# Performance work log

Measured on AMD Instinct MI355X. Metric: run time of the kernel, lower is better.

The kernel has to match this reference:

```python
import jax, jax.numpy as jnp
import numpy as np

EMBED_DIM = 512
NUM_HEADS = 8
HEAD_DIM = EMBED_DIM // NUM_HEADS
REL_MAX = 16
NUM_POS_IDS = 2 * REL_MAX + 1 + 1  # 34 (directed + padding id)
PADDING_IDX = 0
B, S = 2, 2048


def setup_inputs() -> dict:
    key = jax.random.key(0)
    ks = jax.random.split(key, 9)
    Q = jax.random.normal(ks[0], (B, S, EMBED_DIM), dtype=jnp.float32)
    K = jax.random.normal(ks[1], (B, S, EMBED_DIM), dtype=jnp.float32)
    V = jax.random.normal(ks[2], (B, S, EMBED_DIM), dtype=jnp.float32)
    rel_pos_ids = jax.random.randint(ks[3], (B, S, S), 0, NUM_POS_IDS, dtype=jnp.int64) if jax.config.jax_enable_x64 else jax.random.randint(ks[3], (B, S, S), 0, NUM_POS_IDS, dtype=jnp.int32)
    scale = 0.02
    Wq = jax.random.normal(ks[4], (EMBED_DIM, EMBED_DIM), dtype=jnp.float32) * scale
    Wk = jax.random.normal(ks[5], (EMBED_DIM, EMBED_DIM), dtype=jnp.float32) * scale
    Wv = jax.random.normal(ks[6], (EMBED_DIM, EMBED_DIM), dtype=jnp.float32) * scale
    Wo = jax.random.normal(ks[7], (EMBED_DIM, EMBED_DIM), dtype=jnp.float32) * scale
    rel_emb = jax.random.normal(ks[8], (NUM_POS_IDS, EMBED_DIM), dtype=jnp.float32) * scale
    rel_emb = rel_emb.at[PADDING_IDX].set(0.0)  # nn.Embedding padding_idx row is zero
    return {"Q": Q, "K": K, "V": V, "rel_pos_ids": rel_pos_ids,
            "Wq": Wq, "Wk": Wk, "Wv": Wv, "Wo": Wo, "rel_emb": rel_emb}


def _proj(x, W):
    # Linear (no bias) then strided head split: view(B, S, head_dim, H) -> (B, H, S, head_dim)
    b, s, _ = x.shape
    y = x @ W.T
    return y.reshape(b, s, HEAD_DIM, NUM_HEADS).transpose(0, 3, 1, 2)


def _forward(Q, K, V, rel_pos_ids, Wq, Wk, Wv, Wo, rel_emb):
    b, sq, _ = Q.shape
    Qp = _proj(Q, Wq)  # (B, H, Sq, hd)
    Kp = _proj(K, Wk)  # (B, H, Sk, hd)
    Vp = _proj(V, Wv)  # (B, H, Sk, hd)

    # rel_embeds split per head with the same strided layout: (P, hd, H) -> (H, P, hd)
    R = rel_emb.reshape(NUM_POS_IDS, HEAD_DIM, NUM_HEADS).transpose(2, 0, 1)
    # Q_rel: (B, H, Sq, P)
    Q_rel = jnp.einsum('bhsd,hpd->bhsp', Qp, R)
    # gather per-pair relative bias: (B, H, Sq, Sk)
    rel_shift = jnp.take_along_axis(Q_rel, rel_pos_ids[:, None, :, :], axis=3)
    mask = (rel_pos_ids == PADDING_IDX)[:, None, :, :]
    rel_shift = jnp.where(mask, -jnp.inf, rel_shift)

    energy = (jnp.einsum('bhqd,bhkd->bhqk', Qp, Kp) + rel_shift) / jnp.sqrt(jnp.float32(HEAD_DIM))
    attn = jax.nn.softmax(energy, axis=-1)
    out = jnp.einsum('bhqk,bhkd->bhqd', attn, Vp)  # (B, H, Sq, hd)
    # inverse of strided split: (B, Sq, hd, H) -> flatten last two
    out = out.transpose(0, 2, 3, 1).reshape(b, sq, EMBED_DIM)
    return out @ Wo.T


def reference(Q, K, V, rel_pos_ids, Wq, Wk, Wv, Wo, rel_emb):
    return _forward(Q, K, V, rel_pos_ids, Wq, Wk, Wv, Wo, rel_emb)
```

## Files before the change

kernel.cpp:

```cpp
#include <hip/hip_runtime.h>
#include <cstdint>
#include <cstddef>

#define SEQ   2048
#define BBAT  2
#define EMBED 512
#define NH    8
#define HD    64
#define NPOS  34

typedef __bf16 bf16;
typedef __bf16 bf16x8 __attribute__((ext_vector_type(8)));
typedef float  f32x4  __attribute__((ext_vector_type(4)));
typedef int    int32x4 __attribute__((ext_vector_type(4)));

#define ESCALE 0.1803368801111204f

__device__ __forceinline__ f32x4 mfma16(bf16x8 a, bf16x8 b, f32x4 c){
  return __builtin_amdgcn_mfma_f32_16x16x32_bf16(a, b, c, 0, 0, 0);
}

__device__ __forceinline__ void barrier_lgkm(){
  asm volatile("s_waitcnt lgkmcnt(0)" ::: "memory");
  __builtin_amdgcn_s_barrier();
  __builtin_amdgcn_sched_barrier(0);
}

__global__ __launch_bounds__(256) void k_prep(
    const float* __restrict__ Q, const float* __restrict__ K, const float* __restrict__ V,
    const float* __restrict__ Wq, const float* __restrict__ Wk,
    const float* __restrict__ Wv, const float* __restrict__ Wo,
    const float* __restrict__ RE,
    bf16* __restrict__ Qb, bf16* __restrict__ Kb, bf16* __restrict__ Vb,
    bf16* __restrict__ Wall, bf16* __restrict__ Rb)
{
  const int NCONV = 3*524288;
  const int NW = 196608, NO = 262144;
  int i = blockIdx.x*256 + threadIdx.x;
  if (i < NCONV){
    int tsel = i >> 19, j = i & 524287;
    const float* s = tsel==0 ? Q : (tsel==1 ? K : V);
    bf16* d       = tsel==0 ? Qb : (tsel==1 ? Kb : Vb);
    float4 v = ((const float4*)s)[j];
    union { bf16 e[4]; ushort4 u; } pk;
    pk.e[0]=(bf16)v.x; pk.e[1]=(bf16)v.y; pk.e[2]=(bf16)v.z; pk.e[3]=(bf16)v.w;
    ((ushort4*)d)[j] = pk.u;
  } else {
    int j = i - NCONV;
    if (j < NW){
      int w  = j >> 16;
      int r  = j & 65535;
      int np = r >> 7, c4 = (r & 127) << 2;
      const float* W = (w==0) ? Wq : ((w==1) ? Wk : Wv);
      int src = ((np & 63) << 3) + (np >> 6);
      float4 v = *(const float4*)(W + (size_t)src*512 + c4);
      union { bf16 e[4]; ushort4 u; } pk;
      pk.e[0]=(bf16)v.x; pk.e[1]=(bf16)v.y; pk.e[2]=(bf16)v.z; pk.e[3]=(bf16)v.w;
      *(ushort4*)(Wall + (size_t)w*262144 + (size_t)np*512 + c4) = pk.u;
    } else if (j < NW + NO){
      int jj = j - NW;
      int n = jj >> 9, kp = jj & 511;
      int src = ((kp & 63) << 3) + (kp >> 6);
      Wall[(size_t)3*262144 + (size_t)n*512 + kp] = (bf16)Wo[(size_t)n*512 + src];
    } else {
      int jj = j - NW - NO;
      if (jj < 8*48*64){
        int h  = jj / (48*64);
        int r2 = jj - h*(48*64);
        int p  = r2 >> 6, dd = r2 & 63;
        float v = (p < NPOS) ? RE[(size_t)p*512 + dd*8 + h] : 0.f;
        Rb[jj] = (bf16)v;
      }
    }
  }
}

__global__ __launch_bounds__(256,2) void k_gemm_proj(
    const bf16* __restrict__ Qb, const bf16* __restrict__ Kb, const bf16* __restrict__ Vb,
    const bf16* __restrict__ W,  bf16* __restrict__ Qp, bf16* __restrict__ Kp, bf16* __restrict__ Vt)
{
  const bf16* A  = blockIdx.z==0 ? Qb : (blockIdx.z==1 ? Kb : Vb);
  const bf16* Bw = W + (size_t)blockIdx.z*262144;

  __shared__ __align__(16) bf16 As[128][72];
  __shared__ __align__(16) bf16 Bs[64][72];
  const int t = threadIdx.x;
  const int w = t >> 6, lane = t & 63, l15 = lane & 15, quad = lane >> 4;
  const int wm = (w & 1) * 64, wn = (w >> 1) * 32;
  const int m0 = blockIdx.y * 128, n0 = blockIdx.x * 64;

  f32x4 acc[4][2];
  #pragma unroll
  for (int mt=0; mt<4; ++mt)
    #pragma unroll
    for (int nt=0; nt<2; ++nt) acc[mt][nt] = (f32x4){0.f,0.f,0.f,0.f};

  for (int kt = 0; kt < 512; kt += 64){
    #pragma unroll
    for (int i = 0; i < 4; ++i){
      int lin = t + 256*i;
      int r = lin >> 3, c8 = (lin & 7) << 3;
      *(uint4*)&As[r][c8] = *(const uint4*)(A + (size_t)(m0 + r)*512 + kt + c8);
    }
    #pragma unroll
    for (int i = 0; i < 2; ++i){
      int lin = t + 256*i;
      int r = lin >> 3, c8 = (lin & 7) << 3;
      *(uint4*)&Bs[r][c8] = *(const uint4*)(Bw + (size_t)(n0 + r)*512 + kt + c8);
    }
    __syncthreads();
    #pragma unroll
    for (int ks = 0; ks < 2; ++ks){
      bf16x8 am[4], bn[2];
      #pragma unroll
      for (int x=0;x<4;++x) am[x] = *(const bf16x8*)&As[wm + x*16 + l15][ks*32 + quad*8];
      #pragma unroll
      for (int y=0;y<2;++y) bn[y] = *(const bf16x8*)&Bs[wn + y*16 + l15][ks*32 + quad*8];
      #pragma unroll
      for (int mt=0;mt<4;++mt)
        #pragma unroll
        for (int nt=0;nt<2;++nt)
          acc[mt][nt] = mfma16(am[mt], bn[nt], acc[mt][nt]);
    }
    __syncthreads();
  }

  if (blockIdx.z != 2){
    bf16* C = blockIdx.z==0 ? Qp : Kp;
    const float scl = (blockIdx.z==0) ? ESCALE : 1.0f;
    #pragma unroll
    for (int mt=0;mt<4;++mt)
      #pragma unroll
      for (int r=0;r<4;++r){
        int m = m0 + wm + mt*16 + quad*4 + r;
        #pragma unroll
        for (int nt=0;nt<2;++nt)
          C[(size_t)m*512 + n0 + wn + nt*16 + l15] = (bf16)(acc[mt][nt][r] * scl);
      }
  } else {
    bf16 (*VT)[136] = (bf16(*)[136])As;
    #pragma unroll
    for (int mt=0;mt<4;++mt)
      #pragma unroll
      for (int r=0;r<4;++r){
        int m = wm + mt*16 + quad*4 + r;
        #pragma unroll
        for (int nt=0;nt<2;++nt)
          VT[wn + nt*16 + l15][m] = (bf16)acc[mt][nt][r];
      }
    __syncthreads();
    const int h = blockIdx.x, b = m0 >> 11, s0 = m0 & 2047;
    const int n = t >> 2, c0 = (t & 3) * 32;
    bf16* dst = Vt + ((size_t)((b*NH + h)*HD + n))*SEQ + s0 + c0;
    #pragma unroll
    for (int i = 0; i < 4; ++i)
      *(uint4*)(dst + i*8) = *(const uint4*)&VT[n][c0 + i*8];
  }
}

__global__ __launch_bounds__(256,2) void k_gemm_out(
    const bf16* __restrict__ A, const bf16* __restrict__ Bw, float* __restrict__ C)
{
  __shared__ __align__(16) bf16 As[64][72];
  __shared__ __align__(16) bf16 Bs[64][72];
  const int t = threadIdx.x;
  const int w = t >> 6, lane = t & 63, l15 = lane & 15, quad = lane >> 4;
  const int wm = (w & 1) * 32, wn = (w >> 1) * 32;
  const int m0 = blockIdx.y * 64, n0 = blockIdx.x * 64;

  f32x4 acc[2][2];
  #pragma unroll
  for (int mt=0; mt<2; ++mt)
    #pragma unroll
    for (int nt=0; nt<2; ++nt) acc[mt][nt] = (f32x4){0.f,0.f,0.f,0.f};

  for (int kt = 0; kt < 512; kt += 64){
    #pragma unroll
    for (int i = 0; i < 2; ++i){
      int lin = t + 256*i;
      int r = lin >> 3, c8 = (lin & 7) << 3;
      *(uint4*)&As[r][c8] = *(const uint4*)(A  + (size_t)(m0 + r)*512 + kt + c8);
      *(uint4*)&Bs[r][c8] = *(const uint4*)(Bw + (size_t)(n0 + r)*512 + kt + c8);
    }
    __syncthreads();
    #pragma unroll
    for (int ks = 0; ks < 2; ++ks){
      bf16x8 am[2], bn[2];
      #pragma unroll
      for (int x=0;x<2;++x) am[x] = *(const bf16x8*)&As[wm + x*16 + l15][ks*32 + quad*8];
      #pragma unroll
      for (int y=0;y<2;++y) bn[y] = *(const bf16x8*)&Bs[wn + y*16 + l15][ks*32 + quad*8];
      #pragma unroll
      for (int mt=0;mt<2;++mt)
        #pragma unroll
        for (int nt=0;nt<2;++nt)
          acc[mt][nt] = mfma16(am[mt], bn[nt], acc[mt][nt]);
    }
    __syncthreads();
  }
  #pragma unroll
  for (int mt=0;mt<2;++mt)
    #pragma unroll
    for (int r=0;r<4;++r){
      int m = m0 + wm + mt*16 + quad*4 + r;
      #pragma unroll
      for (int nt=0;nt<2;++nt)
        C[(size_t)m*512 + n0 + wn + nt*16 + l15] = acc[mt][nt][r];
    }
}

__global__ __launch_bounds__(256,2) void k_attn(
    const bf16* __restrict__ Qp, const bf16* __restrict__ Kp,
    const bf16* __restrict__ Vt, const bf16* __restrict__ Rb,
    const int* __restrict__ ids, bf16* __restrict__ Out)
{
  __shared__ __align__(16) bf16 Ks[128][72];
  __shared__ __align__(16) bf16 Vs[64][136];
  __shared__ __align__(16) bf16 Ps[64][136];
  __shared__ float lutT[35][65];
  __shared__ float lsum_s[128];

  const int t = threadIdx.x;
  const int b = blockIdx.z, h = blockIdx.y;
  const int q0 = blockIdx.x * 64;
  const int w = t >> 6, lane = t & 63, l15 = lane & 15, quad = lane >> 4;
  const int qh = w & 1, kh = w >> 1;

  const size_t idb = (size_t)b*SEQ*SEQ;
  const bf16* kbase = Kp + (size_t)b*SEQ*EMBED + h*HD;
  const bf16* vbase = Vt + (size_t)(b*NH + h)*HD*SEQ;

  const int krow = t >> 3, kcol = (t & 7) << 3;
  const int vrow = t >> 4, vcol = (t & 15) << 3;

  uint4 ka0, ka1, ka2, ka3, va0, va1, va2, va3;
  uint4 kb0, kb1, kb2, kb3, vb0, vb1, vb2, vb3;
  ka0 = *(const uint4*)(kbase + (size_t)(krow     )*EMBED + kcol);
  ka1 = *(const uint4*)(kbase + (size_t)(krow + 32)*EMBED + kcol);
  ka2 = *(const uint4*)(kbase + (size_t)(krow + 64)*EMBED + kcol);
  ka3 = *(const uint4*)(kbase + (size_t)(krow + 96)*EMBED + kcol);
  va0 = *(const uint4*)(vbase + (size_t)(vrow     )*SEQ + vcol);
  va1 = *(const uint4*)(vbase + (size_t)(vrow + 16)*SEQ + vcol);
  va2 = *(const uint4*)(vbase + (size_t)(vrow + 32)*SEQ + vcol);
  va3 = *(const uint4*)(vbase + (size_t)(vrow + 48)*SEQ + vcol);

  int32x4 nid[2][4];
  #pragma unroll
  for (int mt=0; mt<2; ++mt)
    #pragma unroll
    for (int nt=0; nt<4; ++nt)
      nid[mt][nt] = *(const int32x4*)(ids + idb
          + (size_t)(q0 + qh*32 + mt*16 + l15)*SEQ
          + kh*64 + nt*16 + quad*4);

  {
    const bf16* qbrow = Qp + (size_t)(b*SEQ + q0 + w*16 + l15)*EMBED + h*HD;
    bf16x8 ab0 = *(const bf16x8*)(qbrow + quad*8);
    bf16x8 ab1 = *(const bf16x8*)(qbrow + 32 + quad*8);
    const bf16* rh = Rb + h*3072;
    #pragma unroll
    for (int nt = 0; nt < 3; ++nt){
      bf16x8 r0 = *(const bf16x8*)(rh + (nt*16 + l15)*64 + quad*8);
      bf16x8 r1 = *(const bf16x8*)(rh + (nt*16 + l15)*64 + 32 + quad*8);
      f32x4 c = (f32x4){0.f,0.f,0.f,0.f};
      c = mfma16(ab0, r0, c);
      c = mfma16(ab1, r1, c);
      int p = nt*16 + l15;
      if (p < NPOS){
        #pragma unroll
        for (int r = 0; r < 4; ++r)
          lutT[p][w*16 + quad*4 + r] = (p == 0) ? -1e30f : c[r];
      }
    }
  }

  bf16x8 bq[2][2];
  #pragma unroll
  for (int mt = 0; mt < 2; ++mt){
    const bf16* qrow = Qp + (size_t)(b*SEQ + q0 + qh*32 + mt*16 + l15)*EMBED + h*HD;
    bq[mt][0] = *(const bf16x8*)(qrow + quad*8);
    bq[mt][1] = *(const bf16x8*)(qrow + 32 + quad*8);
  }

  f32x4 acc[2][4];
  #pragma unroll
  for (int mt=0;mt<2;++mt)
    #pragma unroll
    for (int nt=0;nt<4;++nt) acc[mt][nt] = (f32x4){0.f,0.f,0.f,0.f};
  float lsum[2] = {0.f, 0.f};

#define ATTN_BODY(KT, K0,K1,K2,K3, V0,V1,V2,V3, L0,L1,L2,L3, M0,M1,M2,M3)       \
  {                                                                             \
    barrier_lgkm();              \
    *(uint4*)&Ks[krow     ][kcol] = K0;                                         \
    *(uint4*)&Ks[krow + 32][kcol] = K1;                                         \
    *(uint4*)&Ks[krow + 64][kcol] = K2;                                         \
    *(uint4*)&Ks[krow + 96][kcol] = K3;                                         \
    *(uint4*)&Vs[vrow     ][vcol] = V0;                                         \
    *(uint4*)&Vs[vrow + 16][vcol] = V1;                                         \
    *(uint4*)&Vs[vrow + 32][vcol] = V2;                                         \
    *(uint4*)&Vs[vrow + 48][vcol] = V3;                                         \
    if ((KT) < 15){                                                             \
      const bf16* kp2 = kbase + (size_t)(((KT)+1)*128)*EMBED + kcol;            \
      const bf16* vp2 = vbase + ((KT)+1)*128 + vcol;                            \
      L0 = *(const uint4*)(kp2 + (size_t)(krow     )*EMBED);                    \
      L1 = *(const uint4*)(kp2 + (size_t)(krow + 32)*EMBED);                    \
      L2 = *(const uint4*)(kp2 + (size_t)(krow + 64)*EMBED);                    \
      L3 = *(const uint4*)(kp2 + (size_t)(krow + 96)*EMBED);                    \
      M0 = *(const uint4*)(vp2 + (size_t)(vrow     )*SEQ);                      \
      M1 = *(const uint4*)(vp2 + (size_t)(vrow + 16)*SEQ);                      \
      M2 = *(const uint4*)(vp2 + (size_t)(vrow + 32)*SEQ);                      \
      M3 = *(const uint4*)(vp2 + (size_t)(vrow + 48)*SEQ);                      \
    }                                                                           \
    barrier_lgkm();                \
    float wvv[2][4][4];                                                         \
    _Pragma("unroll")                                                           \
    for (int mt = 0; mt < 2; ++mt){                                             \
      const float* lcol = &lutT[0][qh*32 + mt*16 + l15];                        \
      _Pragma("unroll")                                                         \
      for (int nt = 0; nt < 4; ++nt){                                           \
        int32x4 v = nid[mt][nt];                                                \
        wvv[mt][nt][0] = lcol[v[0] * 65];                                       \
        wvv[mt][nt][1] = lcol[v[1] * 65];                                       \
        wvv[mt][nt][2] = lcol[v[2] * 65];                                       \
        wvv[mt][nt][3] = lcol[v[3] * 65];                                       \
      }                                                                         \
    }                                                                           \
    if ((KT) < 15){                                                             \
      _Pragma("unroll")                                                         \
      for (int mt = 0; mt < 2; ++mt)                                            \
        _Pragma("unroll")                                                       \
        for (int nt = 0; nt < 4; ++nt)                                          \
          nid[mt][nt] = *(const int32x4*)(ids + idb                             \
              + (size_t)(q0 + qh*32 + mt*16 + l15)*SEQ                          \
              + (((KT)+1)*128) + kh*64 + nt*16 + quad*4);                       \
    }                                                                           \
    f32x4 sf[2][4];                                                             \
    __builtin_amdgcn_s_setprio(1);                                              \
    _Pragma("unroll")                                                           \
    for (int nt = 0; nt < 4; ++nt){                                             \
      bf16x8 ak0 = *(const bf16x8*)&Ks[kh*64 + nt*16 + l15][quad*8];            \
      bf16x8 ak1 = *(const bf16x8*)&Ks[kh*64 + nt*16 + l15][32 + quad*8];       \
      _Pragma("unroll")                                                         \
      for (int mt = 0; mt < 2; ++mt){                                           \
        f32x4 c = (f32x4){0.f,0.f,0.f,0.f};                                     \
        c = mfma16(ak0, bq[mt][0], c);                                          \
        c = mfma16(ak1, bq[mt][1], c);                                          \
        sf[mt][nt] = c;                                                         \
      }                                                                         \
    }                                                                           \
    __builtin_amdgcn_s_setprio(0);                                              \
    _Pragma("unroll")                                                           \
    for (int mt = 0; mt < 2; ++mt){                                             \
      _Pragma("unroll")                                                         \
      for (int nt = 0; nt < 4; ++nt){                                           \
        union { bf16 e[4]; uint2 u; } pk;                                       \
        float p0 = __builtin_amdgcn_exp2f(sf[mt][nt][0] + wvv[mt][nt][0]);      \
        float p1 = __builtin_amdgcn_exp2f(sf[mt][nt][1] + wvv[mt][nt][1]);      \
        float p2 = __builtin_amdgcn_exp2f(sf[mt][nt][2] + wvv[mt][nt][2]);      \
        float p3 = __builtin_amdgcn_exp2f(sf[mt][nt][3] + wvv[mt][nt][3]);      \
        pk.e[0] = (bf16)p0; pk.e[1] = (bf16)p1;                                 \
        pk.e[2] = (bf16)p2; pk.e[3] = (bf16)p3;                                 \
        lsum[mt] += (p0 + p1) + (p2 + p3);                                      \
        *(uint2*)&Ps[qh*32 + mt*16 + l15][kh*64 + nt*16 + quad*4] = pk.u;       \
      }                                                                         \
    }                                                                           \
    __builtin_amdgcn_s_setprio(1);                                              \
    _Pragma("unroll")                                                           \
    for (int ks = 0; ks < 2; ++ks){                                             \
      bf16x8 ap[2];                                                             \
      _Pragma("unroll")                                                         \
      for (int mt = 0; mt < 2; ++mt)                                            \
        ap[mt] = *(const bf16x8*)&Ps[qh*32 + mt*16 + l15][kh*64 + ks*32 + quad*8]; \
      _Pragma("unroll")                                                         \
      for (int nt = 0; nt < 4; ++nt){                                           \
        bf16x8 bv = *(const bf16x8*)&Vs[nt*16 + l15][kh*64 + ks*32 + quad*8];   \
        _Pragma("unroll")                                                       \
        for (int mt = 0; mt < 2; ++mt)                                          \
          acc[mt][nt] = mfma16(ap[mt], bv, acc[mt][nt]);                        \
      }                                                                         \
    }                                                                           \
    __builtin_amdgcn_s_setprio(0);                                              \
  }

  for (int kt2 = 0; kt2 < 16; kt2 += 2){
    ATTN_BODY(kt2,     ka0,ka1,ka2,ka3, va0,va1,va2,va3, kb0,kb1,kb2,kb3, vb0,vb1,vb2,vb3)
    ATTN_BODY(kt2 + 1, kb0,kb1,kb2,kb3, vb0,vb1,vb2,vb3, ka0,ka1,ka2,ka3, va0,va1,va2,va3)
  }
#undef ATTN_BODY

  __syncthreads();

  #pragma unroll
  for (int mt = 0; mt < 2; ++mt){
    float v = lsum[mt];
    v += __shfl_xor(v, 16);
    v += __shfl_xor(v, 32);
    if (quad == 0) lsum_s[kh*64 + qh*32 + mt*16 + l15] = v;
  }

  float* xch = (float*)&Ps[0][0];
  if (kh == 1){
    #pragma unroll
    for (int mt = 0; mt < 2; ++mt)
      #pragma unroll
      for (int nt = 0; nt < 4; ++nt){
        f32x4 a = acc[mt][nt];
        #pragma unroll
        for (int r = 0; r < 4; ++r)
          xch[(qh*32 + mt*16 + quad*4 + r)*65 + nt*16 + l15] = a[r];
      }
  }
  __syncthreads();

  if (kh == 0){
    #pragma unroll
    for (int mt = 0; mt < 2; ++mt){
      #pragma unroll
      for (int r = 0; r < 4; ++r){
        int ql = qh*32 + mt*16 + quad*4 + r;
        float inv = __builtin_amdgcn_rcpf(lsum_s[ql] + lsum_s[64 + ql]);
        #pragma unroll
        for (int nt = 0; nt < 4; ++nt){
          float o = acc[mt][nt][r] + xch[ql*65 + nt*16 + l15];
          Out[(size_t)(b*SEQ + q0 + ql)*EMBED + h*HD + nt*16 + l15] = (bf16)(o*inv);
        }
      }
    }
  }
}

extern "C" void kernel_launch(void* const* d_in, const int* in_sizes, int n_in,
                              void* d_out, int out_size, void* d_ws, size_t ws_size,
                              hipStream_t stream)
{
  (void)in_sizes; (void)n_in; (void)out_size;
  const float* Q  = (const float*)d_in[0];
  const float* K  = (const float*)d_in[1];
  const float* V  = (const float*)d_in[2];
  const int*   ID = (const int*)d_in[3];
  const float* Wq = (const float*)d_in[4];
  const float* Wk = (const float*)d_in[5];
  const float* Wv = (const float*)d_in[6];
  const float* Wo = (const float*)d_in[7];
  const float* RE = (const float*)d_in[8];
  float* out = (float*)d_out;

  const size_t MB = (size_t)1 << 20;
  if (ws_size < 36*MB) return;
  char* ws = (char*)d_ws;
  bf16*  Qb    = (bf16*)(ws + 0*MB);
  bf16*  Kb    = (bf16*)(ws + 4*MB);
  bf16*  Vb    = (bf16*)(ws + 8*MB);
  bf16*  Qp    = (bf16*)(ws + 12*MB);
  bf16*  Kp    = (bf16*)(ws + 16*MB);
  bf16*  Vt    = (bf16*)(ws + 20*MB);
  bf16*  Wall  = (bf16*)(ws + 24*MB);
  bf16*  Wop   = Wall + (size_t)3*262144;
  bf16*  Rb    = (bf16*)(ws + 26*MB);
  bf16*  AO    = (bf16*)(ws + 0*MB);

  k_prep      <<<dim3(8032),    256, 0, stream>>>(Q, K, V, Wq, Wk, Wv, Wo, RE,
                                                  Qb, Kb, Vb, Wall, Rb);
  k_gemm_proj <<<dim3(8,32,3),  256, 0, stream>>>(Qb, Kb, Vb, Wall, Qp, Kp, Vt);
  k_attn      <<<dim3(32,8,2),  256, 0, stream>>>(Qp, Kp, Vt, Rb, ID, AO);
  k_gemm_out  <<<dim3(8,64),    256, 0, stream>>>(AO, Wop, out);
}
```

Measured before the change: 184.1 us.

## Fuse four kernels into one persistent cooperative megakernel with grid syncs

Replaces the four separate launches (prep, projection GEMM, attention, output GEMM) with a single cooperative kernel of 512 workgroups that runs each stage in turn, separated by grid-wide syncs. It is meant to remove per-launch overhead and the gaps between kernels. In exchange, every stage is forced onto a fixed 512-block grid at occupancy 2, and the stages are duplicated code. If the cooperative launch fails, it falls back to the original four launches.

```diff
diff --git a/kernel.cpp b/kernel.cpp
--- a/kernel.cpp
+++ b/kernel.cpp
@@ -1,6 +1,9 @@
 #include <hip/hip_runtime.h>
+#include <hip/hip_cooperative_groups.h>
 #include <cstdint>
 #include <cstddef>
+
+namespace cg = cooperative_groups;
 
 #define SEQ   2048
 #define BBAT  2
@@ -25,6 +28,7 @@
   __builtin_amdgcn_s_barrier();
   __builtin_amdgcn_sched_barrier(0);
 }
+
 
 __global__ __launch_bounds__(256) void k_prep(
     const float* __restrict__ Q, const float* __restrict__ K, const float* __restrict__ V,
@@ -291,7 +295,7 @@
 
 #define ATTN_BODY(KT, K0,K1,K2,K3, V0,V1,V2,V3, L0,L1,L2,L3, M0,M1,M2,M3)       \
   {                                                                             \
-    barrier_lgkm();              \
+    barrier_lgkm();                                                             \
     *(uint4*)&Ks[krow     ][kcol] = K0;                                         \
     *(uint4*)&Ks[krow + 32][kcol] = K1;                                         \
     *(uint4*)&Ks[krow + 64][kcol] = K2;                                         \
@@ -312,7 +316,7 @@
       M2 = *(const uint4*)(vp2 + (size_t)(vrow + 32)*SEQ);                      \
       M3 = *(const uint4*)(vp2 + (size_t)(vrow + 48)*SEQ);                      \
     }                                                                           \
-    barrier_lgkm();                \
+    barrier_lgkm();                                                             \
     float wvv[2][4][4];                                                         \
     _Pragma("unroll")                                                           \
     for (int mt = 0; mt < 2; ++mt){                                             \
@@ -427,6 +431,419 @@
         }
       }
     }
+  }
+}
+
+__global__ __launch_bounds__(256,2) void k_mega(
+    const float* Q, const float* K, const float* V,
+    const int*   ids,
+    const float* Wq, const float* Wk, const float* Wv, const float* Wo,
+    const float* RE,
+    bf16* Qb, bf16* Kb, bf16* Vb,
+    bf16* Wall, bf16* Rb,
+    bf16* Qp, bf16* Kp, bf16* Vt,
+    bf16* AO, float* out)
+{
+  __shared__ __align__(16) char smem[62864];
+  cg::grid_group grid = cg::this_grid();
+  const int t = threadIdx.x;
+  const int wg = blockIdx.x;
+
+  {
+    const int NCONV = 3*524288;
+    const int NW = 196608, NO = 262144;
+    for (int blk = wg; blk < 8032; blk += 512){
+      int i = blk*256 + t;
+      if (i < NCONV){
+        int tsel = i >> 19, j = i & 524287;
+        const float* s = tsel==0 ? Q : (tsel==1 ? K : V);
+        bf16* d       = tsel==0 ? Qb : (tsel==1 ? Kb : Vb);
+        float4 v = ((const float4*)s)[j];
+        union { bf16 e[4]; ushort4 u; } pk;
+        pk.e[0]=(bf16)v.x; pk.e[1]=(bf16)v.y; pk.e[2]=(bf16)v.z; pk.e[3]=(bf16)v.w;
+        ((ushort4*)d)[j] = pk.u;
+      } else {
+        int j = i - NCONV;
+        if (j < NW){
+          int w2 = j >> 16;
+          int r  = j & 65535;
+          int np = r >> 7, c4 = (r & 127) << 2;
+          const float* W = (w2==0) ? Wq : ((w2==1) ? Wk : Wv);
+          int src = ((np & 63) << 3) + (np >> 6);
+          float4 v = *(const float4*)(W + (size_t)src*512 + c4);
+          union { bf16 e[4]; ushort4 u; } pk;
+          pk.e[0]=(bf16)v.x; pk.e[1]=(bf16)v.y; pk.e[2]=(bf16)v.z; pk.e[3]=(bf16)v.w;
+          *(ushort4*)(Wall + (size_t)w2*262144 + (size_t)np*512 + c4) = pk.u;
+        } else if (j < NW + NO){
+          int jj = j - NW;
+          int n = jj >> 9, kp = jj & 511;
+          int src = ((kp & 63) << 3) + (kp >> 6);
+          Wall[(size_t)3*262144 + (size_t)n*512 + kp] = (bf16)Wo[(size_t)n*512 + src];
+        } else {
+          int jj = j - NW - NO;
+          if (jj < 8*48*64){
+            int h2 = jj / (48*64);
+            int r2 = jj - h2*(48*64);
+            int p  = r2 >> 6, dd = r2 & 63;
+            float v = (p < NPOS) ? RE[(size_t)p*512 + dd*8 + h2] : 0.f;
+            Rb[jj] = (bf16)v;
+          }
+        }
+      }
+    }
+  }
+  grid.sync();
+
+  {
+    bf16 (*As)[72] = (bf16(*)[72])smem;
+    bf16 (*Bs)[72] = (bf16(*)[72])(smem + 18432);
+    const int w = t >> 6, lane = t & 63, l15 = lane & 15, quad = lane >> 4;
+    const int wm = (w & 1) * 64, wn = (w >> 1) * 32;
+
+    for (int tile = wg; tile < 768; tile += 512){
+      const int z  = tile >> 8;
+      const int by = (tile & 255) >> 3, bx = tile & 7;
+      const bf16* A  = z==0 ? Qb : (z==1 ? Kb : Vb);
+      const bf16* Bw = Wall + (size_t)z*262144;
+      const int m0 = by * 128, n0 = bx * 64;
+
+      __syncthreads();
+
+      f32x4 acc[4][2];
+      #pragma unroll
+      for (int mt=0; mt<4; ++mt)
+        #pragma unroll
+        for (int nt=0; nt<2; ++nt) acc[mt][nt] = (f32x4){0.f,0.f,0.f,0.f};
+
+      for (int kt = 0; kt < 512; kt += 64){
+        #pragma unroll
+        for (int i = 0; i < 4; ++i){
+          int lin = t + 256*i;
+          int r = lin >> 3, c8 = (lin & 7) << 3;
+          *(uint4*)&As[r][c8] = *(const uint4*)(A + (size_t)(m0 + r)*512 + kt + c8);
+        }
+        #pragma unroll
+        for (int i = 0; i < 2; ++i){
+          int lin = t + 256*i;
+          int r = lin >> 3, c8 = (lin & 7) << 3;
+          *(uint4*)&Bs[r][c8] = *(const uint4*)(Bw + (size_t)(n0 + r)*512 + kt + c8);
+        }
+        __syncthreads();
+        #pragma unroll
+        for (int ks = 0; ks < 2; ++ks){
+          bf16x8 am[4], bn[2];
+          #pragma unroll
+          for (int x=0;x<4;++x) am[x] = *(const bf16x8*)&As[wm + x*16 + l15][ks*32 + quad*8];
+          #pragma unroll
+          for (int y=0;y<2;++y) bn[y] = *(const bf16x8*)&Bs[wn + y*16 + l15][ks*32 + quad*8];
+          #pragma unroll
+          for (int mt=0;mt<4;++mt)
+            #pragma unroll
+            for (int nt=0;nt<2;++nt)
+              acc[mt][nt] = mfma16(am[mt], bn[nt], acc[mt][nt]);
+        }
+        __syncthreads();
+      }
+
+      if (z != 2){
+        bf16* C = z==0 ? Qp : Kp;
+        const float scl = (z==0) ? ESCALE : 1.0f;
+        #pragma unroll
+        for (int mt=0;mt<4;++mt)
+          #pragma unroll
+          for (int r=0;r<4;++r){
+            int m = m0 + wm + mt*16 + quad*4 + r;
+            #pragma unroll
+            for (int nt=0;nt<2;++nt)
+              C[(size_t)m*512 + n0 + wn + nt*16 + l15] = (bf16)(acc[mt][nt][r] * scl);
+          }
+      } else {
+        bf16 (*VT)[136] = (bf16(*)[136])As;
+        #pragma unroll
+        for (int mt=0;mt<4;++mt)
+          #pragma unroll
+          for (int r=0;r<4;++r){
+            int m = wm + mt*16 + quad*4 + r;
+            #pragma unroll
+            for (int nt=0;nt<2;++nt)
+              VT[wn + nt*16 + l15][m] = (bf16)acc[mt][nt][r];
+          }
+        __syncthreads();
+        const int h = bx, b = m0 >> 11, s0 = m0 & 2047;
+        const int n = t >> 2, c0 = (t & 3) * 32;
+        bf16* dst = Vt + ((size_t)((b*NH + h)*HD + n))*SEQ + s0 + c0;
+        #pragma unroll
+        for (int i = 0; i < 4; ++i)
+          *(uint4*)(dst + i*8) = *(const uint4*)&VT[n][c0 + i*8];
+      }
+    }
+  }
+  grid.sync();
+
+  {
+    bf16 (*Ks)[72]   = (bf16(*)[72])smem;
+    bf16 (*Vs)[136]  = (bf16(*)[136])(smem + 18432);
+    bf16 (*Ps)[136]  = (bf16(*)[136])(smem + 35840);
+    float (*lutT)[65]= (float(*)[65])(smem + 53248);
+    float *lsum_s    = (float*)(smem + 62348);
+
+    const int b = wg >> 8, h = (wg >> 5) & 7;
+    const int q0 = (wg & 31) * 64;
+    const int w = t >> 6, lane = t & 63, l15 = lane & 15, quad = lane >> 4;
+    const int qh = w & 1, kh = w >> 1;
+
+    const size_t idb = (size_t)b*SEQ*SEQ;
+    const bf16* kbase = Kp + (size_t)b*SEQ*EMBED + h*HD;
+    const bf16* vbase = Vt + (size_t)(b*NH + h)*HD*SEQ;
+
+    const int krow = t >> 3, kcol = (t & 7) << 3;
+    const int vrow = t >> 4, vcol = (t & 15) << 3;
+
+    uint4 ka0, ka1, ka2, ka3, va0, va1, va2, va3;
+    uint4 kb0, kb1, kb2, kb3, vb0, vb1, vb2, vb3;
+    ka0 = *(const uint4*)(kbase + (size_t)(krow     )*EMBED + kcol);
+    ka1 = *(const uint4*)(kbase + (size_t)(krow + 32)*EMBED + kcol);
+    ka2 = *(const uint4*)(kbase + (size_t)(krow + 64)*EMBED + kcol);
+    ka3 = *(const uint4*)(kbase + (size_t)(krow + 96)*EMBED + kcol);
+    va0 = *(const uint4*)(vbase + (size_t)(vrow     )*SEQ + vcol);
+    va1 = *(const uint4*)(vbase + (size_t)(vrow + 16)*SEQ + vcol);
+    va2 = *(const uint4*)(vbase + (size_t)(vrow + 32)*SEQ + vcol);
+    va3 = *(const uint4*)(vbase + (size_t)(vrow + 48)*SEQ + vcol);
+
+    int32x4 nid[2][4];
+    #pragma unroll
+    for (int mt=0; mt<2; ++mt)
+      #pragma unroll
+      for (int nt=0; nt<4; ++nt)
+        nid[mt][nt] = *(const int32x4*)(ids + idb
+            + (size_t)(q0 + qh*32 + mt*16 + l15)*SEQ
+            + kh*64 + nt*16 + quad*4);
+
+    {
+      const bf16* qbrow = Qp + (size_t)(b*SEQ + q0 + w*16 + l15)*EMBED + h*HD;
+      bf16x8 ab0 = *(const bf16x8*)(qbrow + quad*8);
+      bf16x8 ab1 = *(const bf16x8*)(qbrow + 32 + quad*8);
+      const bf16* rh = Rb + h*3072;
+      #pragma unroll
+      for (int nt = 0; nt < 3; ++nt){
+        bf16x8 r0 = *(const bf16x8*)(rh + (nt*16 + l15)*64 + quad*8);
+        bf16x8 r1 = *(const bf16x8*)(rh + (nt*16 + l15)*64 + 32 + quad*8);
+        f32x4 c = (f32x4){0.f,0.f,0.f,0.f};
+        c = mfma16(ab0, r0, c);
+        c = mfma16(ab1, r1, c);
+        int p = nt*16 + l15;
+        if (p < NPOS){
+          #pragma unroll
+          for (int r = 0; r < 4; ++r)
+            lutT[p][w*16 + quad*4 + r] = (p == 0) ? -1e30f : c[r];
+        }
+      }
+    }
+
+    bf16x8 bq[2][2];
+    #pragma unroll
+    for (int mt = 0; mt < 2; ++mt){
+      const bf16* qrow = Qp + (size_t)(b*SEQ + q0 + qh*32 + mt*16 + l15)*EMBED + h*HD;
+      bq[mt][0] = *(const bf16x8*)(qrow + quad*8);
+      bq[mt][1] = *(const bf16x8*)(qrow + 32 + quad*8);
+    }
+
+    f32x4 acc[2][4];
+    #pragma unroll
+    for (int mt=0;mt<2;++mt)
+      #pragma unroll
+      for (int nt=0;nt<4;++nt) acc[mt][nt] = (f32x4){0.f,0.f,0.f,0.f};
+    float lsum[2] = {0.f, 0.f};
+
+#define ATTN_BODY(KT, K0,K1,K2,K3, V0,V1,V2,V3, L0,L1,L2,L3, M0,M1,M2,M3)       \
+  {                                                                             \
+    barrier_lgkm();                                                             \
+    *(uint4*)&Ks[krow     ][kcol] = K0;                                         \
+    *(uint4*)&Ks[krow + 32][kcol] = K1;                                         \
+    *(uint4*)&Ks[krow + 64][kcol] = K2;                                         \
+    *(uint4*)&Ks[krow + 96][kcol] = K3;                                         \
+    *(uint4*)&Vs[vrow     ][vcol] = V0;                                         \
+    *(uint4*)&Vs[vrow + 16][vcol] = V1;                                         \
+    *(uint4*)&Vs[vrow + 32][vcol] = V2;                                         \
+    *(uint4*)&Vs[vrow + 48][vcol] = V3;                                         \
+    if ((KT) < 15){                                                             \
+      const bf16* kp2 = kbase + (size_t)(((KT)+1)*128)*EMBED + kcol;            \
+      const bf16* vp2 = vbase + ((KT)+1)*128 + vcol;                            \
+      L0 = *(const uint4*)(kp2 + (size_t)(krow     )*EMBED);                    \
+      L1 = *(const uint4*)(kp2 + (size_t)(krow + 32)*EMBED);                    \
+      L2 = *(const uint4*)(kp2 + (size_t)(krow + 64)*EMBED);                    \
+      L3 = *(const uint4*)(kp2 + (size_t)(krow + 96)*EMBED);                    \
+      M0 = *(const uint4*)(vp2 + (size_t)(vrow     )*SEQ);                      \
+      M1 = *(const uint4*)(vp2 + (size_t)(vrow + 16)*SEQ);                      \
+      M2 = *(const uint4*)(vp2 + (size_t)(vrow + 32)*SEQ);                      \
+      M3 = *(const uint4*)(vp2 + (size_t)(vrow + 48)*SEQ);                      \
+    }                                                                           \
+    barrier_lgkm();                                                             \
+    float wvv[2][4][4];                                                         \
+    _Pragma("unroll")                                                           \
+    for (int mt = 0; mt < 2; ++mt){                                             \
+      const float* lcol = &lutT[0][qh*32 + mt*16 + l15];                        \
+      _Pragma("unroll")                                                         \
+      for (int nt = 0; nt < 4; ++nt){                                           \
+        int32x4 v = nid[mt][nt];                                                \
+        wvv[mt][nt][0] = lcol[v[0] * 65];                                       \
+        wvv[mt][nt][1] = lcol[v[1] * 65];                                       \
+        wvv[mt][nt][2] = lcol[v[2] * 65];                                       \
+        wvv[mt][nt][3] = lcol[v[3] * 65];                                       \
+      }                                                                         \
+    }                                                                           \
+    if ((KT) < 15){                                                             \
+      _Pragma("unroll")                                                         \
+      for (int mt = 0; mt < 2; ++mt)                                            \
+        _Pragma("unroll")                                                       \
+        for (int nt = 0; nt < 4; ++nt)                                          \
+          nid[mt][nt] = *(const int32x4*)(ids + idb                             \
+              + (size_t)(q0 + qh*32 + mt*16 + l15)*SEQ                          \
+              + (((KT)+1)*128) + kh*64 + nt*16 + quad*4);                       \
+    }                                                                           \
+    f32x4 sf[2][4];                                                             \
+    __builtin_amdgcn_s_setprio(1);                                              \
+    _Pragma("unroll")                                                           \
+    for (int nt = 0; nt < 4; ++nt){                                             \
+      bf16x8 ak0 = *(const bf16x8*)&Ks[kh*64 + nt*16 + l15][quad*8];            \
+      bf16x8 ak1 = *(const bf16x8*)&Ks[kh*64 + nt*16 + l15][32 + quad*8];       \
+      _Pragma("unroll")                                                         \
+      for (int mt = 0; mt < 2; ++mt){                                           \
+        f32x4 c = (f32x4){0.f,0.f,0.f,0.f};                                     \
+        c = mfma16(ak0, bq[mt][0], c);                                          \
+        c = mfma16(ak1, bq[mt][1], c);                                          \
+        sf[mt][nt] = c;                                                         \
+      }                                                                         \
+    }                                                                           \
+    __builtin_amdgcn_s_setprio(0);                                              \
+    _Pragma("unroll")                                                           \
+    for (int mt = 0; mt < 2; ++mt){                                             \
+      _Pragma("unroll")                                                         \
+      for (int nt = 0; nt < 4; ++nt){                                           \
+        union { bf16 e[4]; uint2 u; } pk;                                       \
+        float p0 = __builtin_amdgcn_exp2f(sf[mt][nt][0] + wvv[mt][nt][0]);      \
+        float p1 = __builtin_amdgcn_exp2f(sf[mt][nt][1] + wvv[mt][nt][1]);      \
+        float p2 = __builtin_amdgcn_exp2f(sf[mt][nt][2] + wvv[mt][nt][2]);      \
+        float p3 = __builtin_amdgcn_exp2f(sf[mt][nt][3] + wvv[mt][nt][3]);      \
+        pk.e[0] = (bf16)p0; pk.e[1] = (bf16)p1;                                 \
+        pk.e[2] = (bf16)p2; pk.e[3] = (bf16)p3;                                 \
+        lsum[mt] += (p0 + p1) + (p2 + p3);                                      \
+        *(uint2*)&Ps[qh*32 + mt*16 + l15][kh*64 + nt*16 + quad*4] = pk.u;       \
+      }                                                                         \
+    }                                                                           \
+    __builtin_amdgcn_s_setprio(1);                                              \
+    _Pragma("unroll")                                                           \
+    for (int ks = 0; ks < 2; ++ks){                                             \
+      bf16x8 ap[2];                                                             \
+      _Pragma("unroll")                                                         \
+      for (int mt = 0; mt < 2; ++mt)                                            \
+        ap[mt] = *(const bf16x8*)&Ps[qh*32 + mt*16 + l15][kh*64 + ks*32 + quad*8]; \
+      _Pragma("unroll")                                                         \
+      for (int nt = 0; nt < 4; ++nt){                                           \
+        bf16x8 bv = *(const bf16x8*)&Vs[nt*16 + l15][kh*64 + ks*32 + quad*8];   \
+        _Pragma("unroll")                                                       \
+        for (int mt = 0; mt < 2; ++mt)                                          \
+          acc[mt][nt] = mfma16(ap[mt], bv, acc[mt][nt]);                        \
+      }                                                                         \
+    }                                                                           \
+    __builtin_amdgcn_s_setprio(0);                                              \
+  }
+
+    for (int kt2 = 0; kt2 < 16; kt2 += 2){
+      ATTN_BODY(kt2,     ka0,ka1,ka2,ka3, va0,va1,va2,va3, kb0,kb1,kb2,kb3, vb0,vb1,vb2,vb3)
+      ATTN_BODY(kt2 + 1, kb0,kb1,kb2,kb3, vb0,vb1,vb2,vb3, ka0,ka1,ka2,ka3, va0,va1,va2,va3)
+    }
+#undef ATTN_BODY
+
+    __syncthreads();
+
+    #pragma unroll
+    for (int mt = 0; mt < 2; ++mt){
+      float v = lsum[mt];
+      v += __shfl_xor(v, 16);
+      v += __shfl_xor(v, 32);
+      if (quad == 0) lsum_s[kh*64 + qh*32 + mt*16 + l15] = v;
+    }
+
+    float* xch = (float*)&Ps[0][0];
+    if (kh == 1){
+      #pragma unroll
+      for (int mt = 0; mt < 2; ++mt)
+        #pragma unroll
+        for (int nt = 0; nt < 4; ++nt){
+          f32x4 a = acc[mt][nt];
+          #pragma unroll
+          for (int r = 0; r < 4; ++r)
+            xch[(qh*32 + mt*16 + quad*4 + r)*65 + nt*16 + l15] = a[r];
+        }
+    }
+    __syncthreads();
+
+    if (kh == 0){
+      #pragma unroll
+      for (int mt = 0; mt < 2; ++mt){
+        #pragma unroll
+        for (int r = 0; r < 4; ++r){
+          int ql = qh*32 + mt*16 + quad*4 + r;
+          float inv = __builtin_amdgcn_rcpf(lsum_s[ql] + lsum_s[64 + ql]);
+          #pragma unroll
+          for (int nt = 0; nt < 4; ++nt){
+            float o = acc[mt][nt][r] + xch[ql*65 + nt*16 + l15];
+            AO[(size_t)(b*SEQ + q0 + ql)*EMBED + h*HD + nt*16 + l15] = (bf16)(o*inv);
+          }
+        }
+      }
+    }
+  }
+  grid.sync();
+
+  {
+    bf16 (*As)[72] = (bf16(*)[72])smem;
+    bf16 (*Bs)[72] = (bf16(*)[72])(smem + 9216);
+    const bf16* Bw = Wall + (size_t)3*262144;
+    const int w = t >> 6, lane = t & 63, l15 = lane & 15, quad = lane >> 4;
+    const int wm = (w & 1) * 32, wn = (w >> 1) * 32;
+    const int m0 = (wg >> 3) * 64, n0 = (wg & 7) * 64;
+
+    f32x4 acc[2][2];
+    #pragma unroll
+    for (int mt=0; mt<2; ++mt)
+      #pragma unroll
+      for (int nt=0; nt<2; ++nt) acc[mt][nt] = (f32x4){0.f,0.f,0.f,0.f};
+
+    for (int kt = 0; kt < 512; kt += 64){
+      #pragma unroll
+      for (int i = 0; i < 2; ++i){
+        int lin = t + 256*i;
+        int r = lin >> 3, c8 = (lin & 7) << 3;
+        *(uint4*)&As[r][c8] = *(const uint4*)(AO + (size_t)(m0 + r)*512 + kt + c8);
+        *(uint4*)&Bs[r][c8] = *(const uint4*)(Bw + (size_t)(n0 + r)*512 + kt + c8);
+      }
+      __syncthreads();
+      #pragma unroll
+      for (int ks = 0; ks < 2; ++ks){
+        bf16x8 am[2], bn[2];
+        #pragma unroll
+        for (int x=0;x<2;++x) am[x] = *(const bf16x8*)&As[wm + x*16 + l15][ks*32 + quad*8];
+        #pragma unroll
+        for (int y=0;y<2;++y) bn[y] = *(const bf16x8*)&Bs[wn + y*16 + l15][ks*32 + quad*8];
+        #pragma unroll
+        for (int mt=0;mt<2;++mt)
+          #pragma unroll
+          for (int nt=0;nt<2;++nt)
+            acc[mt][nt] = mfma16(am[mt], bn[nt], acc[mt][nt]);
+      }
+      __syncthreads();
+    }
+    #pragma unroll
+    for (int mt=0;mt<2;++mt)
+      #pragma unroll
+      for (int r=0;r<4;++r){
+        int m = m0 + wm + mt*16 + quad*4 + r;
+        #pragma unroll
+        for (int nt=0;nt<2;++nt)
+          out[(size_t)m*512 + n0 + wn + nt*16 + l15] = acc[mt][nt][r];
+      }
   }
 }
 
@@ -460,9 +877,21 @@
   bf16*  Rb    = (bf16*)(ws + 26*MB);
   bf16*  AO    = (bf16*)(ws + 0*MB);
 
-  k_prep      <<<dim3(8032),    256, 0, stream>>>(Q, K, V, Wq, Wk, Wv, Wo, RE,
-                                                  Qb, Kb, Vb, Wall, Rb);
-  k_gemm_proj <<<dim3(8,32,3),  256, 0, stream>>>(Qb, Kb, Vb, Wall, Qp, Kp, Vt);
-  k_attn      <<<dim3(32,8,2),  256, 0, stream>>>(Qp, Kp, Vt, Rb, ID, AO);
-  k_gemm_out  <<<dim3(8,64),    256, 0, stream>>>(AO, Wop, out);
+  void* args[] = {
+    (void*)&Q, (void*)&K, (void*)&V, (void*)&ID,
+    (void*)&Wq, (void*)&Wk, (void*)&Wv, (void*)&Wo, (void*)&RE,
+    (void*)&Qb, (void*)&Kb, (void*)&Vb,
+    (void*)&Wall, (void*)&Rb,
+    (void*)&Qp, (void*)&Kp, (void*)&Vt,
+    (void*)&AO, (void*)&out
+  };
+  hipError_t err = hipLaunchCooperativeKernel((void*)k_mega, dim3(512), dim3(256),
+                                              args, 0, stream);
+  if (err != hipSuccess){
+    k_prep      <<<dim3(8032),    256, 0, stream>>>(Q, K, V, Wq, Wk, Wv, Wo, RE,
+                                                    Qb, Kb, Vb, Wall, Rb);
+    k_gemm_proj <<<dim3(8,32,3),  256, 0, stream>>>(Qb, Kb, Vb, Wall, Qp, Kp, Vt);
+    k_attn      <<<dim3(32,8,2),  256, 0, stream>>>(Qp, Kp, Vt, Rb, ID, AO);
+    k_gemm_out  <<<dim3(8,64),    256, 0, stream>>>(AO, Wop, out);
+  }
 }
```

Measured after the change: 392.0 us. +112.9%, slower.

## Fuse fp32-to-bf16 conversion into projection GEMM and drop prep kernel

Applied to the files above, without the earlier changes.

Removes the separate prep kernel. The projection GEMM now loads fp32 Q/K/V and the weights directly and converts them to bf16 while staging into shared memory. Wo is permuted and converted by an extra z-slice of blocks in the same launch, and the relative embeddings are read and converted inside the attention kernel. The output GEMM is retiled to 128-row blocks. This saves one launch and the bf16 intermediate round trip, at the cost of doubling global read bytes in the GEMM's inner loop.

```diff
diff --git a/kernel.cpp b/kernel.cpp
--- a/kernel.cpp
+++ b/kernel.cpp
@@ -26,62 +26,125 @@
   __builtin_amdgcn_sched_barrier(0);
 }
 
-__global__ __launch_bounds__(256) void k_prep(
-    const float* __restrict__ Q, const float* __restrict__ K, const float* __restrict__ V,
-    const float* __restrict__ Wq, const float* __restrict__ Wk,
-    const float* __restrict__ Wv, const float* __restrict__ Wo,
-    const float* __restrict__ RE,
-    bf16* __restrict__ Qb, bf16* __restrict__ Kb, bf16* __restrict__ Vb,
-    bf16* __restrict__ Wall, bf16* __restrict__ Rb)
+__global__ __launch_bounds__(256,2) void k_proj(
+    const float* __restrict__ Qf, const float* __restrict__ Kf, const float* __restrict__ Vf,
+    const float* __restrict__ Wq, const float* __restrict__ Wk, const float* __restrict__ Wv,
+    const float* __restrict__ Wo,
+    bf16* __restrict__ Qp, bf16* __restrict__ Kp, bf16* __restrict__ Vt,
+    bf16* __restrict__ Wop)
 {
-  const int NCONV = 3*524288;
-  const int NW = 196608, NO = 262144;
-  int i = blockIdx.x*256 + threadIdx.x;
-  if (i < NCONV){
-    int tsel = i >> 19, j = i & 524287;
-    const float* s = tsel==0 ? Q : (tsel==1 ? K : V);
-    bf16* d       = tsel==0 ? Qb : (tsel==1 ? Kb : Vb);
-    float4 v = ((const float4*)s)[j];
+  const int z = blockIdx.z;
+  const int t = threadIdx.x;
+
+  if (z == 3){
+    int base = (blockIdx.y*8 + blockIdx.x)*1024 + t*4;
+    int n = base >> 9, kp = base & 511;
     union { bf16 e[4]; ushort4 u; } pk;
-    pk.e[0]=(bf16)v.x; pk.e[1]=(bf16)v.y; pk.e[2]=(bf16)v.z; pk.e[3]=(bf16)v.w;
-    ((ushort4*)d)[j] = pk.u;
+    #pragma unroll
+    for (int j = 0; j < 4; ++j){
+      int kpj = kp + j;
+      int src = ((kpj & 63) << 3) + (kpj >> 6);
+      pk.e[j] = (bf16)Wo[(size_t)n*512 + src];
+    }
+    *(ushort4*)(Wop + (size_t)n*512 + kp) = pk.u;
+    return;
+  }
+
+  const float* A  = z==0 ? Qf : (z==1 ? Kf : Vf);
+  const float* Bw = z==0 ? Wq : (z==1 ? Wk : Wv);
+
+  __shared__ __align__(16) bf16 As[128][72];
+  __shared__ __align__(16) bf16 Bs[64][72];
+  const int w = t >> 6, lane = t & 63, l15 = lane & 15, quad = lane >> 4;
+  const int wm = (w & 1) * 64, wn = (w >> 1) * 32;
+  const int m0 = blockIdx.y * 128, n0 = blockIdx.x * 64;
+
+  f32x4 acc[4][2];
+  #pragma unroll
+  for (int mt=0; mt<4; ++mt)
+    #pragma unroll
+    for (int nt=0; nt<2; ++nt) acc[mt][nt] = (f32x4){0.f,0.f,0.f,0.f};
+
+  for (int kt = 0; kt < 512; kt += 64){
+    #pragma unroll
+    for (int i = 0; i < 4; ++i){
+      int lin = t + 256*i;
+      int r = lin >> 3, c8 = (lin & 7) << 3;
+      const float* src = A + (size_t)(m0 + r)*512 + kt + c8;
+      float4 f0 = *(const float4*)(src);
+      float4 f1 = *(const float4*)(src + 4);
+      union { bf16 e[8]; uint4 u; } pk;
+      pk.e[0]=(bf16)f0.x; pk.e[1]=(bf16)f0.y; pk.e[2]=(bf16)f0.z; pk.e[3]=(bf16)f0.w;
+      pk.e[4]=(bf16)f1.x; pk.e[5]=(bf16)f1.y; pk.e[6]=(bf16)f1.z; pk.e[7]=(bf16)f1.w;
+      *(uint4*)&As[r][c8] = pk.u;
+    }
+    #pragma unroll
+    for (int i = 0; i < 2; ++i){
+      int lin = t + 256*i;
+      int r = lin >> 3, c8 = (lin & 7) << 3;
+      int np = n0 + r;
+      int srcrow = ((np & 63) << 3) + (np >> 6);
+      const float* src = Bw + (size_t)srcrow*512 + kt + c8;
+      float4 f0 = *(const float4*)(src);
+      float4 f1 = *(const float4*)(src + 4);
+      union { bf16 e[8]; uint4 u; } pk;
+      pk.e[0]=(bf16)f0.x; pk.e[1]=(bf16)f0.y; pk.e[2]=(bf16)f0.z; pk.e[3]=(bf16)f0.w;
+      pk.e[4]=(bf16)f1.x; pk.e[5]=(bf16)f1.y; pk.e[6]=(bf16)f1.z; pk.e[7]=(bf16)f1.w;
+      *(uint4*)&Bs[r][c8] = pk.u;
+    }
+    __syncthreads();
+    #pragma unroll
+    for (int ks = 0; ks < 2; ++ks){
+      bf16x8 am[4], bn[2];
+      #pragma unroll
+      for (int x=0;x<4;++x) am[x] = *(const bf16x8*)&As[wm + x*16 + l15][ks*32 + quad*8];
+      #pragma unroll
+      for (int y=0;y<2;++y) bn[y] = *(const bf16x8*)&Bs[wn + y*16 + l15][ks*32 + quad*8];
+      #pragma unroll
+      for (int mt=0;mt<4;++mt)
+        #pragma unroll
+        for (int nt=0;nt<2;++nt)
+          acc[mt][nt] = mfma16(am[mt], bn[nt], acc[mt][nt]);
+    }
+    __syncthreads();
+  }
+
+  if (z != 2){
+    bf16* C = z==0 ? Qp : Kp;
+    const float scl = (z==0) ? ESCALE : 1.0f;
+    #pragma unroll
+    for (int mt=0;mt<4;++mt)
+      #pragma unroll
+      for (int r=0;r<4;++r){
+        int m = m0 + wm + mt*16 + quad*4 + r;
+        #pragma unroll
+        for (int nt=0;nt<2;++nt)
+          C[(size_t)m*512 + n0 + wn + nt*16 + l15] = (bf16)(acc[mt][nt][r] * scl);
+      }
   } else {
-    int j = i - NCONV;
-    if (j < NW){
-      int w  = j >> 16;
-      int r  = j & 65535;
-      int np = r >> 7, c4 = (r & 127) << 2;
-      const float* W = (w==0) ? Wq : ((w==1) ? Wk : Wv);
-      int src = ((np & 63) << 3) + (np >> 6);
-      float4 v = *(const float4*)(W + (size_t)src*512 + c4);
-      union { bf16 e[4]; ushort4 u; } pk;
-      pk.e[0]=(bf16)v.x; pk.e[1]=(bf16)v.y; pk.e[2]=(bf16)v.z; pk.e[3]=(bf16)v.w;
-      *(ushort4*)(Wall + (size_t)w*262144 + (size_t)np*512 + c4) = pk.u;
-    } else if (j < NW + NO){
-      int jj = j - NW;
-      int n = jj >> 9, kp = jj & 511;
-      int src = ((kp & 63) << 3) + (kp >> 6);
-      Wall[(size_t)3*262144 + (size_t)n*512 + kp] = (bf16)Wo[(size_t)n*512 + src];
-    } else {
-      int jj = j - NW - NO;
-      if (jj < 8*48*64){
-        int h  = jj / (48*64);
-        int r2 = jj - h*(48*64);
-        int p  = r2 >> 6, dd = r2 & 63;
-        float v = (p < NPOS) ? RE[(size_t)p*512 + dd*8 + h] : 0.f;
-        Rb[jj] = (bf16)v;
-      }
-    }
-  }
-}
-
-__global__ __launch_bounds__(256,2) void k_gemm_proj(
-    const bf16* __restrict__ Qb, const bf16* __restrict__ Kb, const bf16* __restrict__ Vb,
-    const bf16* __restrict__ W,  bf16* __restrict__ Qp, bf16* __restrict__ Kp, bf16* __restrict__ Vt)
+    bf16 (*VT)[136] = (bf16(*)[136])As;
+    #pragma unroll
+    for (int mt=0;mt<4;++mt)
+      #pragma unroll
+      for (int r=0;r<4;++r){
+        int m = wm + mt*16 + quad*4 + r;
+        #pragma unroll
+        for (int nt=0;nt<2;++nt)
+          VT[wn + nt*16 + l15][m] = (bf16)acc[mt][nt][r];
+      }
+    __syncthreads();
+    const int h = blockIdx.x, b = m0 >> 11, s0 = m0 & 2047;
+    const int n = t >> 2, c0 = (t & 3) * 32;
+    bf16* dst = Vt + ((size_t)((b*NH + h)*HD + n))*SEQ + s0 + c0;
+    #pragma unroll
+    for (int i = 0; i < 4; ++i)
+      *(uint4*)(dst + i*8) = *(const uint4*)&VT[n][c0 + i*8];
+  }
+}
+
+__global__ __launch_bounds__(256,2) void k_gemm_out(
+    const bf16* __restrict__ A, const bf16* __restrict__ Bw, float* __restrict__ C)
 {
-  const bf16* A  = blockIdx.z==0 ? Qb : (blockIdx.z==1 ? Kb : Vb);
-  const bf16* Bw = W + (size_t)blockIdx.z*262144;
-
   __shared__ __align__(16) bf16 As[128][72];
   __shared__ __align__(16) bf16 Bs[64][72];
   const int t = threadIdx.x;
@@ -124,82 +187,8 @@
     }
     __syncthreads();
   }
-
-  if (blockIdx.z != 2){
-    bf16* C = blockIdx.z==0 ? Qp : Kp;
-    const float scl = (blockIdx.z==0) ? ESCALE : 1.0f;
-    #pragma unroll
-    for (int mt=0;mt<4;++mt)
-      #pragma unroll
-      for (int r=0;r<4;++r){
-        int m = m0 + wm + mt*16 + quad*4 + r;
-        #pragma unroll
-        for (int nt=0;nt<2;++nt)
-          C[(size_t)m*512 + n0 + wn + nt*16 + l15] = (bf16)(acc[mt][nt][r] * scl);
-      }
-  } else {
-    bf16 (*VT)[136] = (bf16(*)[136])As;
-    #pragma unroll
-    for (int mt=0;mt<4;++mt)
-      #pragma unroll
-      for (int r=0;r<4;++r){
-        int m = wm + mt*16 + quad*4 + r;
-        #pragma unroll
-        for (int nt=0;nt<2;++nt)
-          VT[wn + nt*16 + l15][m] = (bf16)acc[mt][nt][r];
-      }
-    __syncthreads();
-    const int h = blockIdx.x, b = m0 >> 11, s0 = m0 & 2047;
-    const int n = t >> 2, c0 = (t & 3) * 32;
-    bf16* dst = Vt + ((size_t)((b*NH + h)*HD + n))*SEQ + s0 + c0;
-    #pragma unroll
-    for (int i = 0; i < 4; ++i)
-      *(uint4*)(dst + i*8) = *(const uint4*)&VT[n][c0 + i*8];
-  }
-}
-
-__global__ __launch_bounds__(256,2) void k_gemm_out(
-    const bf16* __restrict__ A, const bf16* __restrict__ Bw, float* __restrict__ C)
-{
-  __shared__ __align__(16) bf16 As[64][72];
-  __shared__ __align__(16) bf16 Bs[64][72];
-  const int t = threadIdx.x;
-  const int w = t >> 6, lane = t & 63, l15 = lane & 15, quad = lane >> 4;
-  const int wm = (w & 1) * 32, wn = (w >> 1) * 32;
-  const int m0 = blockIdx.y * 64, n0 = blockIdx.x * 64;
-
-  f32x4 acc[2][2];
-  #pragma unroll
-  for (int mt=0; mt<2; ++mt)
-    #pragma unroll
-    for (int nt=0; nt<2; ++nt) acc[mt][nt] = (f32x4){0.f,0.f,0.f,0.f};
-
-  for (int kt = 0; kt < 512; kt += 64){
-    #pragma unroll
-    for (int i = 0; i < 2; ++i){
-      int lin = t + 256*i;
-      int r = lin >> 3, c8 = (lin & 7) << 3;
-      *(uint4*)&As[r][c8] = *(const uint4*)(A  + (size_t)(m0 + r)*512 + kt + c8);
-      *(uint4*)&Bs[r][c8] = *(const uint4*)(Bw + (size_t)(n0 + r)*512 + kt + c8);
-    }
-    __syncthreads();
-    #pragma unroll
-    for (int ks = 0; ks < 2; ++ks){
-      bf16x8 am[2], bn[2];
-      #pragma unroll
-      for (int x=0;x<2;++x) am[x] = *(const bf16x8*)&As[wm + x*16 + l15][ks*32 + quad*8];
-      #pragma unroll
-      for (int y=0;y<2;++y) bn[y] = *(const bf16x8*)&Bs[wn + y*16 + l15][ks*32 + quad*8];
-      #pragma unroll
-      for (int mt=0;mt<2;++mt)
-        #pragma unroll
-        for (int nt=0;nt<2;++nt)
-          acc[mt][nt] = mfma16(am[mt], bn[nt], acc[mt][nt]);
-    }
-    __syncthreads();
-  }
-  #pragma unroll
-  for (int mt=0;mt<2;++mt)
+  #pragma unroll
+  for (int mt=0;mt<4;++mt)
     #pragma unroll
     for (int r=0;r<4;++r){
       int m = m0 + wm + mt*16 + quad*4 + r;
@@ -211,7 +200,7 @@
 
 __global__ __launch_bounds__(256,2) void k_attn(
     const bf16* __restrict__ Qp, const bf16* __restrict__ Kp,
-    const bf16* __restrict__ Vt, const bf16* __restrict__ Rb,
+    const bf16* __restrict__ Vt, const float* __restrict__ RE,
     const int* __restrict__ ids, bf16* __restrict__ Out)
 {
   __shared__ __align__(16) bf16 Ks[128][72];
@@ -257,15 +246,21 @@
     const bf16* qbrow = Qp + (size_t)(b*SEQ + q0 + w*16 + l15)*EMBED + h*HD;
     bf16x8 ab0 = *(const bf16x8*)(qbrow + quad*8);
     bf16x8 ab1 = *(const bf16x8*)(qbrow + 32 + quad*8);
-    const bf16* rh = Rb + h*3072;
     #pragma unroll
     for (int nt = 0; nt < 3; ++nt){
-      bf16x8 r0 = *(const bf16x8*)(rh + (nt*16 + l15)*64 + quad*8);
-      bf16x8 r1 = *(const bf16x8*)(rh + (nt*16 + l15)*64 + 32 + quad*8);
+      int p = nt*16 + l15;
+      const int   pc = (p < NPOS) ? p : 0;
+      const float fm = (p < NPOS) ? 1.f : 0.f;
+      const float* rrow = RE + (size_t)pc*512 + h;
+      union { bf16 e[8]; bf16x8 v; } r0u, r1u;
+      #pragma unroll
+      for (int j = 0; j < 8; ++j){
+        r0u.e[j] = (bf16)(fm * rrow[(quad*8 + j)*8]);
+        r1u.e[j] = (bf16)(fm * rrow[(32 + quad*8 + j)*8]);
+      }
       f32x4 c = (f32x4){0.f,0.f,0.f,0.f};
-      c = mfma16(ab0, r0, c);
-      c = mfma16(ab1, r1, c);
-      int p = nt*16 + l15;
+      c = mfma16(ab0, r0u.v, c);
+      c = mfma16(ab1, r1u.v, c);
       if (p < NPOS){
         #pragma unroll
         for (int r = 0; r < 4; ++r)
@@ -449,20 +444,14 @@
   const size_t MB = (size_t)1 << 20;
   if (ws_size < 36*MB) return;
   char* ws = (char*)d_ws;
-  bf16*  Qb    = (bf16*)(ws + 0*MB);
-  bf16*  Kb    = (bf16*)(ws + 4*MB);
-  bf16*  Vb    = (bf16*)(ws + 8*MB);
-  bf16*  Qp    = (bf16*)(ws + 12*MB);
-  bf16*  Kp    = (bf16*)(ws + 16*MB);
-  bf16*  Vt    = (bf16*)(ws + 20*MB);
-  bf16*  Wall  = (bf16*)(ws + 24*MB);
-  bf16*  Wop   = Wall + (size_t)3*262144;
-  bf16*  Rb    = (bf16*)(ws + 26*MB);
   bf16*  AO    = (bf16*)(ws + 0*MB);
-
-  k_prep      <<<dim3(8032),    256, 0, stream>>>(Q, K, V, Wq, Wk, Wv, Wo, RE,
-                                                  Qb, Kb, Vb, Wall, Rb);
-  k_gemm_proj <<<dim3(8,32,3),  256, 0, stream>>>(Qb, Kb, Vb, Wall, Qp, Kp, Vt);
-  k_attn      <<<dim3(32,8,2),  256, 0, stream>>>(Qp, Kp, Vt, Rb, ID, AO);
-  k_gemm_out  <<<dim3(8,64),    256, 0, stream>>>(AO, Wop, out);
-}
+  bf16*  Qp    = (bf16*)(ws + 4*MB);
+  bf16*  Kp    = (bf16*)(ws + 8*MB);
+  bf16*  Vt    = (bf16*)(ws + 12*MB);
+  bf16*  Wop   = (bf16*)(ws + 16*MB);
+
+  k_proj      <<<dim3(8,32,4),  256, 0, stream>>>(Q, K, V, Wq, Wk, Wv, Wo,
+                                                  Qp, Kp, Vt, Wop);
+  k_attn      <<<dim3(32,8,2),  256, 0, stream>>>(Qp, Kp, Vt, RE, ID, AO);
+  k_gemm_out  <<<dim3(8,32),    256, 0, stream>>>(AO, Wop, out);
+}
```

Result: slower. 201.8 us (+9.6%).
